# Kernel tuning notes

Hardware: AMD Instinct MI355X
Metric: run time of the kernel (lower is better)

Reference implementation:

```python
import math
import jax, jax.numpy as jnp
import numpy as np

B, H, L = 8, 512, 4096
N = 64 // 2  # d_state//2 complex pairs
DT_MIN, DT_MAX = 1e-3, 0.1


def setup_inputs() -> dict:
    key = jax.random.key(0)
    k_u, k_dt, k_C, k_D, k_W = jax.random.split(key, 5)
    u = jax.random.normal(k_u, (B, H, L), dtype=jnp.float32)
    log_dt = jax.random.uniform(k_dt, (H,), dtype=jnp.float32) * (
        math.log(DT_MAX) - math.log(DT_MIN)) + math.log(DT_MIN)
    log_A_real = jnp.log(0.5 * jnp.ones((H, N), dtype=jnp.float32))
    A_imag = math.pi * jnp.broadcast_to(jnp.arange(N, dtype=jnp.float32), (H, N))
    C = jax.random.normal(k_C, (H, N, 2), dtype=jnp.float32)  # view_as_real of cfloat
    D = jax.random.normal(k_D, (H,), dtype=jnp.float32)
    W_out = jax.random.normal(k_W, (2 * H, H), dtype=jnp.float32) * 0.05  # 1x1 conv weight
    b_out = jnp.zeros((2 * H,), dtype=jnp.float32)
    return {"u": u, "log_dt": log_dt, "log_A_real": log_A_real, "A_imag": A_imag,
            "C": C, "D": D, "W_out": W_out, "b_out": b_out}


def _ssm_kernel(log_dt, log_A_real, A_imag, C, length):
    dt = jnp.exp(log_dt)                             # (H,)
    A = -jnp.exp(log_A_real) + 1j * A_imag           # (H,N) complex
    dtA = A * dt[:, None]                            # (H,N)
    l = jnp.arange(length, dtype=jnp.float32)
    K = jnp.exp(dtA[:, :, None] * l)                 # (H,N,L) complex Vandermonde
    Cc = C[..., 0] + 1j * C[..., 1]                  # (H,N)
    Cs = Cc * (jnp.exp(dtA) - 1.0) / A               # (H,N)
    return 2.0 * jnp.einsum('hn,hnl->hl', Cs, K).real  # (H,L) real kernel


def reference(u, log_dt, log_A_real, A_imag, C, D, W_out, b_out):
    length = u.shape[-1]
    k = _ssm_kernel(log_dt, log_A_real, A_imag, C, length)  # (H,L)
    n_fft = 2 * length
    k_f = jnp.fft.rfft(k, n=n_fft)                   # (H, L+1)
    u_f = jnp.fft.rfft(u, n=n_fft)                   # (B,H,L+1)
    y = jnp.fft.irfft(u_f * k_f, n=n_fft)[..., :length]  # FFT convolution
    y = y + u * D[:, None]                           # D skip connection
    y = jax.nn.gelu(y, approximate=False)            # torch nn.GELU = exact erf
    y = jnp.einsum('oh,bhl->bol', W_out, y) + b_out[:, None]  # 1x1 conv
    a, b = jnp.split(y, 2, axis=-2)                  # GLU over channel dim
    return a * jax.nn.sigmoid(b)
```

## Files before the change

### kernel.cpp

```cpp
#include <hip/hip_runtime.h>
#include <math.h>

constexpr int cB = 8, cH = 512, cL = 4096, cN = 32;
constexpr int cG = 32, cLC = 128;
constexpr int cHN = cH * cN;

constexpr size_t OF_RR  = 0;
constexpr size_t OF_RI  = (size_t)cHN;
constexpr size_t OF_RPR = (size_t)2*cHN;
constexpr size_t OF_RPI = (size_t)3*cHN;
constexpr size_t OF_C2R = (size_t)4*cHN;
constexpr size_t OF_C2I = (size_t)5*cHN;
constexpr size_t OF_DR  = (size_t)6*cHN;
constexpr size_t OF_DI  = (size_t)7*cHN;
constexpr size_t OF_K   = (size_t)8*cHN;
constexpr size_t OF_WP  = OF_K + (size_t)512*128;
constexpr size_t OF_A   = OF_WP + (size_t)1024*512/2;
constexpr size_t OF_V   = OF_A + (size_t)512*128*192/2;
constexpr size_t OF_XP  = OF_V + (size_t)512*64*128/2;
constexpr size_t OF_G   = OF_XP + (size_t)512*256*64/2;
constexpr size_t OF_GT  = OF_A;

typedef __bf16 bf16x8 __attribute__((ext_vector_type(8)));
typedef float  f32x4  __attribute__((ext_vector_type(4)));

static __device__ __forceinline__ ushort f2bf(float x) {
    unsigned u = __float_as_uint(x);
    unsigned r = (u + 0x7fffu + ((u >> 16) & 1u)) >> 16;
    return (ushort)r;
}
static __device__ __forceinline__ float bf2f(ushort v) {
    return __uint_as_float(((unsigned)v) << 16);
}
static __device__ __forceinline__ unsigned pk2(float a, float b) {
    return (unsigned)f2bf(a) | ((unsigned)f2bf(b) << 16);
}
static __device__ __forceinline__ float gelu(float v) {
    return 0.5f * v * (1.0f + erff(v * 0.70710678118654752f));
}
static __device__ __forceinline__ void gload16(const void* g, void* l) {
    __builtin_amdgcn_global_load_lds(
        (const __attribute__((address_space(1))) unsigned*)g,
        (__attribute__((address_space(3))) unsigned*)l, 16, 0, 0);
}

__global__ void k_consts_vmat(const float* __restrict__ log_dt,
                              const float* __restrict__ log_A_real,
                              const float* __restrict__ A_imag,
                              const float* __restrict__ Cin,
                              float* __restrict__ ws,
                              ushort* __restrict__ wsu)
{
    int tid = blockIdx.x * 256 + threadIdx.x;
    if (tid >= cHN) return;
    int h = tid >> 5, n = tid & 31;
    float dt = expf(log_dt[h]);
    float Ar = -expf(log_A_real[tid]);
    float Ai = A_imag[tid];
    float dr = dt * Ar, di = dt * Ai;
    float er = expf(dr);
    float rr = er * cosf(di), ri = er * sinf(di);
    float erL = expf(dr * (float)cLC);
    float diL = di * (float)cLC;
    float rpr = erL * cosf(diL), rpi = erL * sinf(diL);
    float cr = Cin[2*tid], ci = Cin[2*tid+1];
    float nr = rr - 1.0f, ni = ri;
    float inv = 1.0f / (Ar*Ar + Ai*Ai);
    float wr = (nr*Ar + ni*Ai) * inv;
    float wi = (ni*Ar - nr*Ai) * inv;
    float csr = cr*wr - ci*wi;
    float csi = cr*wi + ci*wr;
    ws[OF_RR  + tid] = rr;  ws[OF_RI  + tid] = ri;
    ws[OF_RPR + tid] = rpr; ws[OF_RPI + tid] = rpi;
    ws[OF_C2R + tid] = 2.0f*csr; ws[OF_C2I + tid] = 2.0f*csi;
    ws[OF_DR  + tid] = dr;  ws[OF_DI  + tid] = di;

    float e127 = expf(dr * 127.f), a127 = di * 127.f;
    float pr = e127 * cosf(a127), pi_ = e127 * sinf(a127);
    float rie = expf(-dr);
    float rc = rie * cosf(di), rs = -rie * sinf(di);
    ushort* vre = wsu + 2*OF_V + ((size_t)h*64 + n) * 128;
    ushort* vim = wsu + 2*OF_V + ((size_t)h*64 + 32 + n) * 128;
    for (int j4 = 0; j4 < 128; j4 += 4) {
        ushort4 r4, i4;
        #pragma unroll
        for (int e = 0; e < 4; ++e) {
            ((ushort*)&r4)[e] = f2bf(pr);
            ((ushort*)&i4)[e] = f2bf(pi_);
            float npr = pr*rc - pi_*rs;
            float npi = pr*rs + pi_*rc;
            pr = npr; pi_ = npi;
        }
        *(ushort4*)&vre[j4] = r4;
        *(ushort4*)&vim[j4] = i4;
    }
}

__global__ void k_pack_w(const float* __restrict__ W, ushort* __restrict__ Wp)
{
    int idx = blockIdx.x * 256 + threadIdx.x;
    int base = idx * 4;
    int m = base >> 9;
    int k = base & 511;
    int src = (m & 1) ? (512 + (m >> 1)) : (m >> 1);
    float4 v = *(const float4*)&W[(size_t)src * 512 + k];
    ushort4 o;
    o.x = f2bf(v.x); o.y = f2bf(v.y); o.z = f2bf(v.z); o.w = f2bf(v.w);
    *(ushort4*)&Wp[base] = o;
}

__global__ void k_embt(const float* __restrict__ ws, const float* __restrict__ Dvec,
                       ushort* __restrict__ wsu)
{
    __shared__ float kv[256];
    int t = threadIdx.x;
    int tid = blockIdx.x * 256 + t;
    int h = tid >> 7, l = tid & 127;
    float fl = (float)l, fl1 = (float)(l + 1);
    const float* dr_ = ws + OF_DR + (size_t)h*32;
    const float* di_ = ws + OF_DI + (size_t)h*32;
    const float* c2r_ = ws + OF_C2R + (size_t)h*32;
    const float* c2i_ = ws + OF_C2I + (size_t)h*32;
    ushort* rowA = wsu + 2*OF_A + ((size_t)h*128 + l) * 192;
    float kacc = 0.f;
    for (int n4 = 0; n4 < 32; n4 += 4) {
        ushort4 prq, npq;
        #pragma unroll
        for (int e = 0; e < 4; ++e) {
            int n = n4 + e;
            float dr = dr_[n], di = di_[n], c2r = c2r_[n], c2i = c2i_[n];
            float e0 = expf(dr * fl), a0 = di * fl;
            float c0 = cosf(a0), s0 = sinf(a0);
            kacc += e0 * (c2r*c0 - c2i*s0);
            float e1 = expf(dr * fl1), a1 = di * fl1;
            float c1 = cosf(a1), s1 = sinf(a1);
            ((ushort*)&prq)[e] = f2bf(e1 * (c2r*c1 - c2i*s1));
            ((ushort*)&npq)[e] = f2bf(-e1 * (c2r*s1 + c2i*c1));
        }
        *(ushort4*)&rowA[128 + n4] = prq;
        *(ushort4*)&rowA[160 + n4] = npq;
    }
    kv[t] = kacc;
    __syncthreads();
    const float* krow = kv + ((t >> 7) << 7);
    float Dh = Dvec[h];
    for (int j8 = 0; j8 < 128; j8 += 8) {
        uint4 q;
        unsigned w[4];
        #pragma unroll
        for (int p = 0; p < 4; ++p) {
            int j0 = j8 + 2*p, j1 = j0 + 1;
            float v0 = (j0 <= l) ? krow[l - j0] : 0.f;
            float v1 = (j1 <= l) ? krow[l - j1] : 0.f;
            if (j0 == l) v0 += Dh;
            if (j1 == l) v1 += Dh;
            w[p] = pk2(v0, v1);
        }
        q.x = w[0]; q.y = w[1]; q.z = w[2]; q.w = w[3];
        *(uint4*)&rowA[j8] = q;
    }
}

__global__ __launch_bounds__(1024) void k_conv(const float* __restrict__ u,
                                               const float* __restrict__ ws,
                                               const ushort* __restrict__ wsu,
                                               ushort* __restrict__ g)
{
    __shared__ ushort sh[76800];
    ushort* As = sh;
    ushort* Bs = sh + 25600;
    ushort* Os = sh;

    const int t = threadIdx.x;
    const int h = blockIdx.x;
    const int wave = t >> 6, lane = t & 63;
    const int lm = lane & 15, q = lane >> 4;

    uint4 areg[3];
    const int arow = t >> 3, ac0 = (t & 7) * 24;
    {
        const ushort* Ab = wsu + 2*OF_A + ((size_t)h*128 + arow) * 192 + ac0;
        #pragma unroll
        for (int e = 0; e < 3; ++e) areg[e] = *(const uint4*)&Ab[8*e];
    }
    {
        const int vrow = t >> 4, vc0 = (t & 15) * 8;
        *(uint4*)&As[vrow*200 + vc0] =
            *(const uint4*)(wsu + 2*OF_V + ((size_t)h*64 + vrow) * 128 + vc0);
    }
    {
        const int gc = t >> 2, qt = t & 3;
        const int ub = gc >> 5, uc = gc & 31;
        const float* up = u + ((size_t)(ub*cH + h)) * cL + (size_t)uc*128 + qt*32;
        ushort* d = &Bs[gc * 200 + qt*32];
        #pragma unroll
        for (int e = 0; e < 4; ++e) {
            float4 f0 = *(const float4*)&up[8*e];
            float4 f1 = *(const float4*)&up[8*e + 4];
            uint4 w;
            w.x = pk2(f0.x, f0.y); w.y = pk2(f0.z, f0.w);
            w.z = pk2(f1.x, f1.y); w.w = pk2(f1.z, f1.w);
            *(uint4*)&d[8*e] = w;
        }
    }
    __syncthreads();

    {
        f32x4 accs[4];
        #pragma unroll
        for (int i = 0; i < 4; ++i) accs[i] = (f32x4){0.f,0.f,0.f,0.f};
        #pragma unroll
        for (int j0 = 0; j0 < 128; j0 += 32) {
            bf16x8 vf[4], uf;
            #pragma unroll
            for (int mi = 0; mi < 4; ++mi)
                vf[mi] = *(const bf16x8*)&As[(16*mi + lm) * 200 + j0 + 8*q];
            uf = *(const bf16x8*)&Bs[(16*wave + lm) * 200 + j0 + 8*q];
            #pragma unroll
            for (int mi = 0; mi < 4; ++mi)
                accs[mi] = __builtin_amdgcn_mfma_f32_16x16x32_bf16(vf[mi], uf, accs[mi], 0,0,0);
        }
        const int col = 16*wave + lm;
        #pragma unroll
        for (int mi = 0; mi < 4; ++mi) {
            ushort4 st;
            st.x = f2bf(accs[mi][0]); st.y = f2bf(accs[mi][1]);
            st.z = f2bf(accs[mi][2]); st.w = f2bf(accs[mi][3]);
            *(ushort4*)&Bs[col*200 + 128 + 16*mi + 4*q] = st;
        }
    }
    __syncthreads();

    if (t < 256) {
        const int sb = t >> 5, sn = t & 31;
        float rpr = ws[OF_RPR + (size_t)h*32 + sn];
        float rpi = ws[OF_RPI + (size_t)h*32 + sn];
        float Xr = 0.f, Xi = 0.f;
        ushort* p = &Bs[(sb*32) * 200 + 128 + sn];
        #pragma unroll 4
        for (int c = 0; c < cG; ++c, p += 200) {
            float sr = bf2f(p[0]), si = bf2f(p[32]);
            p[0]  = f2bf(Xr);
            p[32] = f2bf(Xi);
            float nXr = fmaf(rpr, Xr, fmaf(-rpi, Xi, sr));
            float nXi = fmaf(rpr, Xi, fmaf(rpi, Xr, si));
            Xr = nXr; Xi = nXi;
        }
    }
    {
        ushort* d = &As[arow*200 + ac0];
        #pragma unroll
        for (int e = 0; e < 3; ++e) *(uint4*)&d[8*e] = areg[e];
    }
    __syncthreads();

    const int wm = wave & 1, wn = wave >> 1;
    f32x4 acc[4][2];
    #pragma unroll
    for (int i = 0; i < 4; ++i)
        #pragma unroll
        for (int j = 0; j < 2; ++j) acc[i][j] = (f32x4){0.f,0.f,0.f,0.f};

    #pragma unroll
    for (int k0 = 0; k0 < 192; k0 += 32) {
        if ((wm == 0) && (k0 == 64 || k0 == 96)) continue;
        bf16x8 af[4], bfr[2];
        #pragma unroll
        for (int mi = 0; mi < 4; ++mi)
            af[mi] = *(const bf16x8*)&As[(64*wm + 16*mi + lm) * 200 + k0 + 8*q];
        #pragma unroll
        for (int ni = 0; ni < 2; ++ni)
            bfr[ni] = *(const bf16x8*)&Bs[(32*wn + 16*ni + lm) * 200 + k0 + 8*q];
        #pragma unroll
        for (int mi = 0; mi < 4; ++mi)
            #pragma unroll
            for (int ni = 0; ni < 2; ++ni)
                acc[mi][ni] = __builtin_amdgcn_mfma_f32_16x16x32_bf16(af[mi], bfr[ni], acc[mi][ni], 0,0,0);
    }
    __syncthreads();

    #pragma unroll
    for (int ni = 0; ni < 2; ++ni) {
        int gc = 32*wn + 16*ni + lm;
        #pragma unroll
        for (int mi = 0; mi < 4; ++mi) {
            int l = 64*wm + 16*mi + 4*q;
            ushort4 st;
            st.x = f2bf(gelu(acc[mi][ni][0]));
            st.y = f2bf(gelu(acc[mi][ni][1]));
            st.z = f2bf(gelu(acc[mi][ni][2]));
            st.w = f2bf(gelu(acc[mi][ni][3]));
            *(ushort4*)&Os[gc*136 + l] = st;
        }
    }
    __syncthreads();
    {
        const int gc = t >> 2, qt = t & 3;
        const int ob = gc >> 5, oc = gc & 31;
        ushort* grow = g + ((size_t)(ob*cH + h)) * cL + (size_t)oc*128 + qt*32;
        const ushort* s = &Os[gc*136 + qt*32];
        #pragma unroll
        for (int e = 0; e < 4; ++e)
            *(uint4*)&grow[8*e] = *(const uint4*)&s[8*e];
    }
}

__global__ __launch_bounds__(256) void k_transpose(const ushort* __restrict__ gsrc,
                                                   ushort* __restrict__ gT)
{
    __shared__ ushort tile[64 * 64];
    const int t = threadIdx.x;
    const int b  = blockIdx.z;
    const int h0 = blockIdx.y << 6;
    const int l0 = blockIdx.x << 6;
    const ushort* gb = gsrc + ((size_t)b * cH + h0) * cL + l0;
    const int lb = t & 7;
    #pragma unroll
    for (int half = 0; half < 2; ++half) {
        int r = (t >> 3) + half * 32;
        uint4 v = *(const uint4*)&gb[(size_t)r * cL + lb * 8];
        int sb = lb ^ (r & 7) ^ (r >> 3);
        *(uint4*)&tile[r * 64 + sb * 8] = v;
    }
    __syncthreads();
    ushort* gTb = gT + ((size_t)b * cL + l0) * cH + h0;
    #pragma unroll
    for (int half = 0; half < 2; ++half) {
        int l  = (t >> 3) + half * 32;
        int hb = t & 7;
        ushort vals[8];
        #pragma unroll
        for (int e = 0; e < 8; ++e) {
            int r  = hb * 8 + e;
            int sb = (l >> 3) ^ (r & 7) ^ (r >> 3);
            vals[e] = tile[r * 64 + sb * 8 + (l & 7)];
        }
        *(uint4*)&gTb[(size_t)l * cH + hb * 8] = *(uint4*)vals;
    }
}

__global__ __launch_bounds__(256) void k_gemm2(const ushort* __restrict__ Wp,
                                               const float* __restrict__ bias,
                                               const ushort* __restrict__ gT,
                                               float* __restrict__ out)
{
    __shared__ ushort As[2][128 * 32];
    __shared__ ushort Bs[2][128 * 32];
    const int t    = threadIdx.x;
    const int l0   = blockIdx.x * 128;
    const int by   = blockIdx.y;
    const int b    = blockIdx.z;
    const int wave = t >> 6, lane = t & 63;
    const int wm   = wave & 1, wn = wave >> 1;
    const int lm   = lane & 15, q = lane >> 4;

    const int srow = lane >> 2;
    const int scol = (lane & 3) * 8;
    const ushort* Ag = Wp + (size_t)(by * 128) * 512;
    const ushort* Bg = gT + ((size_t)b * cL + l0) * 512;

    f32x4 acc[4][4];
    #pragma unroll
    for (int i = 0; i < 4; ++i)
        #pragma unroll
        for (int j = 0; j < 4; ++j)
            acc[i][j] = (f32x4){0.f, 0.f, 0.f, 0.f};

    auto stage = [&](ushort* Asb, ushort* Bsb, int k0) {
        #pragma unroll
        for (int j = 0; j < 2; ++j) {
            int row = 32*wave + 16*j + srow;
            gload16(Ag + (size_t)row * 512 + k0 + scol,
                    (char*)Asb + wave*2048 + j*1024);
            gload16(Bg + (size_t)row * 512 + k0 + scol,
                    (char*)Bsb + wave*2048 + j*1024);
        }
    };
    auto compute = [&](const ushort* Asb, const ushort* Bsb) {
        bf16x8 af[4], bfr[4];
        #pragma unroll
        for (int mi = 0; mi < 4; ++mi)
            af[mi] = *(const bf16x8*)&Asb[(64*wm + 16*mi + lm) * 32 + 8*q];
        #pragma unroll
        for (int ni = 0; ni < 4; ++ni)
            bfr[ni] = *(const bf16x8*)&Bsb[(64*wn + 16*ni + lm) * 32 + 8*q];
        #pragma unroll
        for (int mi = 0; mi < 4; ++mi)
            #pragma unroll
            for (int ni = 0; ni < 4; ++ni)
                acc[mi][ni] = __builtin_amdgcn_mfma_f32_16x16x32_bf16(af[mi], bfr[ni], acc[mi][ni], 0,0,0);
    };

    stage(As[0], Bs[0], 0);
    __syncthreads();
    int cur = 0;
    for (int ks = 0; ks < 15; ++ks) {
        stage(As[cur ^ 1], Bs[cur ^ 1], (ks + 1) * 32);
        compute(As[cur], Bs[cur]);
        __syncthreads();
        cur ^= 1;
    }
    compute(As[cur], Bs[cur]);

    const int obase = by * 64 + 32 * wm;
    #pragma unroll
    for (int mi = 0; mi < 4; ++mi) {
        #pragma unroll
        for (int p = 0; p < 2; ++p) {
            int o = obase + 8*mi + 2*q + p;
            float ba = bias[o], bb = bias[512 + o];
            float* orow = out + ((size_t)b * cH + o) * cL + l0 + 64*wn + lm;
            #pragma unroll
            for (int ni = 0; ni < 4; ++ni) {
                float av = acc[mi][ni][2*p]     + ba;
                float gv = acc[mi][ni][2*p + 1] + bb;
                orow[16 * ni] = av / (1.f + expf(-gv));
            }
        }
    }
}

extern "C" void kernel_launch(void* const* d_in, const int* in_sizes, int n_in,
                              void* d_out, int out_size, void* d_ws, size_t ws_size,
                              hipStream_t stream)
{
    (void)in_sizes; (void)n_in; (void)out_size; (void)ws_size;
    const float* u          = (const float*)d_in[0];
    const float* log_dt     = (const float*)d_in[1];
    const float* log_A_real = (const float*)d_in[2];
    const float* A_imag     = (const float*)d_in[3];
    const float* C          = (const float*)d_in[4];
    const float* D          = (const float*)d_in[5];
    const float* W          = (const float*)d_in[6];
    const float* bias       = (const float*)d_in[7];
    float* out = (float*)d_out;
    float* ws  = (float*)d_ws;
    ushort* wsu = (ushort*)d_ws;
    ushort* Wp  = wsu + 2*OF_WP;
    ushort* gbf = wsu + 2*OF_G;
    ushort* gTu = wsu + 2*OF_GT;

    hipLaunchKernelGGL(k_consts_vmat, dim3(cHN/256), dim3(256), 0, stream,
                       log_dt, log_A_real, A_imag, C, ws, wsu);
    hipLaunchKernelGGL(k_pack_w, dim3(1024*512/4/256), dim3(256), 0, stream, W, Wp);
    hipLaunchKernelGGL(k_embt, dim3(512*128/256), dim3(256), 0, stream, ws, D, wsu);
    hipLaunchKernelGGL(k_conv, dim3(512), dim3(1024), 0, stream, u, ws, wsu, gbf);
    hipLaunchKernelGGL(k_transpose, dim3(cL/64, cH/64, cB), dim3(256), 0, stream, gbf, gTu);
    hipLaunchKernelGGL(k_gemm2, dim3(cL/128, 1024/128, cB), dim3(256), 0, stream,
                       Wp, bias, gTu, out);
}
```

Before: 263.1 us.

## Split conv kernel per batch half and read V/A operands from global

The conv kernel now runs two 512-thread blocks per head, each covering four batches, instead of one 1024-thread block covering all eight. The V and A matrix fragments for the MFMA stages are loaded straight from global memory rather than staged in shared memory. This cuts shared memory per block from about 150KB to about 50KB, so more blocks can be resident per CU and the grid gets more parallelism. The cost is that each head's A and V matrices are fetched by two blocks, and the fragment loads now depend on L2/cache latency instead of LDS.

```diff
diff --git a/kernel.cpp b/kernel.cpp
--- a/kernel.cpp
+++ b/kernel.cpp
@@ -161,37 +161,25 @@
     }
 }
 
-__global__ __launch_bounds__(1024) void k_conv(const float* __restrict__ u,
-                                               const float* __restrict__ ws,
-                                               const ushort* __restrict__ wsu,
-                                               ushort* __restrict__ g)
-{
-    __shared__ ushort sh[76800];
-    ushort* As = sh;
-    ushort* Bs = sh + 25600;
-    ushort* Os = sh;
-
+__global__ __launch_bounds__(512, 4) void k_conv(const float* __restrict__ u,
+                                                 const float* __restrict__ ws,
+                                                 const ushort* __restrict__ wsu,
+                                                 ushort* __restrict__ g)
+{
+    __shared__ ushort Bs[128 * 200];
     const int t = threadIdx.x;
-    const int h = blockIdx.x;
+    const int bh = blockIdx.x;
+    const int h  = blockIdx.y;
     const int wave = t >> 6, lane = t & 63;
     const int lm = lane & 15, q = lane >> 4;
 
-    uint4 areg[3];
-    const int arow = t >> 3, ac0 = (t & 7) * 24;
-    {
-        const ushort* Ab = wsu + 2*OF_A + ((size_t)h*128 + arow) * 192 + ac0;
-        #pragma unroll
-        for (int e = 0; e < 3; ++e) areg[e] = *(const uint4*)&Ab[8*e];
-    }
-    {
-        const int vrow = t >> 4, vc0 = (t & 15) * 8;
-        *(uint4*)&As[vrow*200 + vc0] =
-            *(const uint4*)(wsu + 2*OF_V + ((size_t)h*64 + vrow) * 128 + vc0);
-    }
+    const ushort* Vb = wsu + 2*OF_V + (size_t)h * 64 * 128;
+    const ushort* Ab = wsu + 2*OF_A + (size_t)h * 128 * 192;
+
     {
         const int gc = t >> 2, qt = t & 3;
-        const int ub = gc >> 5, uc = gc & 31;
-        const float* up = u + ((size_t)(ub*cH + h)) * cL + (size_t)uc*128 + qt*32;
+        const int b = 4*bh + (gc >> 5), uc = gc & 31;
+        const float* up = u + ((size_t)(b*cH + h)) * cL + (size_t)uc*128 + qt*32;
         ushort* d = &Bs[gc * 200 + qt*32];
         #pragma unroll
         for (int e = 0; e < 4; ++e) {
@@ -214,7 +202,7 @@
             bf16x8 vf[4], uf;
             #pragma unroll
             for (int mi = 0; mi < 4; ++mi)
-                vf[mi] = *(const bf16x8*)&As[(16*mi + lm) * 200 + j0 + 8*q];
+                vf[mi] = *(const bf16x8*)&Vb[(16*mi + lm) * 128 + j0 + 8*q];
             uf = *(const bf16x8*)&Bs[(16*wave + lm) * 200 + j0 + 8*q];
             #pragma unroll
             for (int mi = 0; mi < 4; ++mi)
@@ -231,7 +219,7 @@
     }
     __syncthreads();
 
-    if (t < 256) {
+    if (t < 128) {
         const int sb = t >> 5, sn = t & 31;
         float rpr = ws[OF_RPR + (size_t)h*32 + sn];
         float rpi = ws[OF_RPI + (size_t)h*32 + sn];
@@ -247,11 +235,6 @@
             Xr = nXr; Xi = nXi;
         }
     }
-    {
-        ushort* d = &As[arow*200 + ac0];
-        #pragma unroll
-        for (int e = 0; e < 3; ++e) *(uint4*)&d[8*e] = areg[e];
-    }
     __syncthreads();
 
     const int wm = wave & 1, wn = wave >> 1;
@@ -267,7 +250,7 @@
         bf16x8 af[4], bfr[2];
         #pragma unroll
         for (int mi = 0; mi < 4; ++mi)
-            af[mi] = *(const bf16x8*)&As[(64*wm + 16*mi + lm) * 200 + k0 + 8*q];
+            af[mi] = *(const bf16x8*)&Ab[(64*wm + 16*mi + lm) * 192 + k0 + 8*q];
         #pragma unroll
         for (int ni = 0; ni < 2; ++ni)
             bfr[ni] = *(const bf16x8*)&Bs[(32*wn + 16*ni + lm) * 200 + k0 + 8*q];
@@ -279,6 +262,7 @@
     }
     __syncthreads();
 
+    ushort* Os = Bs;
     #pragma unroll
     for (int ni = 0; ni < 2; ++ni) {
         int gc = 32*wn + 16*ni + lm;
@@ -296,8 +280,8 @@
     __syncthreads();
     {
         const int gc = t >> 2, qt = t & 3;
-        const int ob = gc >> 5, oc = gc & 31;
-        ushort* grow = g + ((size_t)(ob*cH + h)) * cL + (size_t)oc*128 + qt*32;
+        const int b = 4*bh + (gc >> 5), oc = gc & 31;
+        ushort* grow = g + ((size_t)(b*cH + h)) * cL + (size_t)oc*128 + qt*32;
         const ushort* s = &Os[gc*136 + qt*32];
         #pragma unroll
         for (int e = 0; e < 4; ++e)
@@ -444,7 +428,7 @@
                        log_dt, log_A_real, A_imag, C, ws, wsu);
     hipLaunchKernelGGL(k_pack_w, dim3(1024*512/4/256), dim3(256), 0, stream, W, Wp);
     hipLaunchKernelGGL(k_embt, dim3(512*128/256), dim3(256), 0, stream, ws, D, wsu);
-    hipLaunchKernelGGL(k_conv, dim3(512), dim3(1024), 0, stream, u, ws, wsu, gbf);
+    hipLaunchKernelGGL(k_conv, dim3(2, 512), dim3(512), 0, stream, u, ws, wsu, gbf);
     hipLaunchKernelGGL(k_transpose, dim3(cL/64, cH/64, cB), dim3(256), 0, stream, gbf, gTu);
     hipLaunchKernelGGL(k_gemm2, dim3(cL/128, 1024/128, cB), dim3(256), 0, stream,
                        Wp, bias, gTu, out);
```

New measurement: 277.4 us. 5.4% more time.
